# Optimization experiments

Hardware: AMD Instinct MI355X
Metric: run time of the kernel (lower is better)

## Reference

```python
import jax, jax.numpy as jnp
import numpy as np

DIM = 1024


def setup_inputs() -> dict:
    key = jax.random.key(0)
    k1, k2, k3 = jax.random.split(key, 3)
    B, N, D = 8, 2048, DIM
    feature1 = jax.random.normal(k1, (B, N, D), dtype=jnp.float32)
    feature2 = jax.random.normal(k2, (B, N, D), dtype=jnp.float32)
    # torch nn.Linear(dim, 3*dim, bias=False); stored here as [D, 3D] for x @ W
    W_qkv = jax.random.normal(k3, (D, 3 * D), dtype=jnp.float32) * (1.0 / np.sqrt(D))
    return {"feature1": feature1, "feature2": feature2, "W_qkv": W_qkv, "topk": 16}


def _qkv(x, W):
    b, n, d = x.shape
    qkv = (x @ W).reshape(b, n, 3, d)  # [B,N,3,D]
    q, k, v = qkv[:, :, 0], qkv[:, :, 1], qkv[:, :, 2]
    return q, k, v


def _topk_renorm(attn, topk):
    # attn: [B,N,N] row-softmax. Keep top-k per row, renormalize by row-sum of
    # the PRE-mask attention (which is 1.0 — faithful to the original code).
    b, n, _ = attn.shape
    _, idx = jax.lax.top_k(attn, topk)  # idx: [B,N,topk]
    bi = jnp.arange(b)[:, None, None]
    ri = jnp.arange(n)[None, :, None]
    mask = jnp.zeros_like(attn).at[bi, ri, idx].set(1.0)
    denom = jnp.sum(attn, axis=2)[:, :, None]  # [B,N,1], == 1 after softmax
    return attn * mask / denom


def reference(feature1, feature2, W_qkv, topk):
    d = feature1.shape[-1]
    scale = 1.0 / d ** 0.5
    q1, k1, v1 = _qkv(feature1, W_qkv)
    q2, k2, v2 = _qkv(feature2, W_qkv)
    dot1 = jnp.einsum("bqd,bkd->bqk", q1, k2) * scale
    dot2 = jnp.einsum("bqd,bkd->bqk", q2, k1) * scale
    attn1 = jax.nn.softmax(dot1, axis=-1)
    attn2 = jax.nn.softmax(dot2, axis=-1)
    attn1 = _topk_renorm(attn1, topk)
    attn2 = _topk_renorm(attn2, topk)
    feature_2to1 = jnp.einsum("bqk,bkd->bqd", attn1, v2)
    feature_1to2 = jnp.einsum("bqk,bkd->bqd", attn2, v1)
    return (feature_2to1, feature_1to2)
```

## Files before the change

kernel.cpp:

```cpp
#include <hip/hip_runtime.h>
#include <hip/hip_bf16.h>
#include <math.h>


#define SEQ 2048
#define DIMD 1024
#define NCAND 24

typedef __bf16 bf16x8 __attribute__((ext_vector_type(8)));
typedef float f32x4 __attribute__((ext_vector_type(4)));

__device__ __forceinline__ void split1(float x, unsigned short& h, unsigned short& l)
{
    __hip_bfloat16 hb = __float2bfloat16(x);
    float hf = __bfloat162float(hb);
    __hip_bfloat16 lb = __float2bfloat16(x - hf);
    h = *reinterpret_cast<unsigned short*>(&hb);
    l = *reinterpret_cast<unsigned short*>(&lb);
}

__global__ __launch_bounds__(256) void k_gemm_m(const float* __restrict__ W,
                                                double* __restrict__ M)
{
    __shared__ double As[16][65];
    __shared__ double Bs[16][65];
    const int tid = threadIdx.x;
    const int tx = tid & 15, ty = tid >> 4;
    const int m0 = blockIdx.x * 64, n0 = blockIdx.y * 64;
    const int lr = tid >> 2;
    const int lk = (tid & 3) * 4;
    double acc[4][4] = {};
    for (int k0 = 0; k0 < 1024; k0 += 16) {
        float4 a = *(const float4*)(W + (size_t)(m0 + lr) * 3072 + k0 + lk);
        As[lk+0][lr] = a.x; As[lk+1][lr] = a.y; As[lk+2][lr] = a.z; As[lk+3][lr] = a.w;
        float4 b = *(const float4*)(W + (size_t)(n0 + lr) * 3072 + 1024 + k0 + lk);
        Bs[lk+0][lr] = b.x; Bs[lk+1][lr] = b.y; Bs[lk+2][lr] = b.z; Bs[lk+3][lr] = b.w;
        __syncthreads();
        #pragma unroll
        for (int kk = 0; kk < 16; ++kk) {
            double av[4], bv[4];
            #pragma unroll
            for (int i = 0; i < 4; ++i) av[i] = As[kk][ty*4+i];
            #pragma unroll
            for (int j = 0; j < 4; ++j) bv[j] = Bs[kk][tx*4+j];
            #pragma unroll
            for (int i = 0; i < 4; ++i)
                #pragma unroll
                for (int j = 0; j < 4; ++j)
                    acc[i][j] = fma(av[i], bv[j], acc[i][j]);
        }
        __syncthreads();
    }
    #pragma unroll
    for (int i = 0; i < 4; ++i)
        #pragma unroll
        for (int j = 0; j < 4; ++j)
            M[(size_t)(m0 + ty*4 + i) * 1024 + n0 + tx*4 + j] = acc[i][j];
}

__global__ __launch_bounds__(256) void k_gemm_y64(const float* __restrict__ X,
                                                  const double* __restrict__ M,
                                                  double* __restrict__ Yd,
                                                  unsigned short* __restrict__ Yh,
                                                  unsigned short* __restrict__ Yl)
{
    __shared__ double As[16][65];
    __shared__ double Bs[16][65];
    const int tid = threadIdx.x;
    const int tx = tid & 15, ty = tid >> 4;
    const int m0 = blockIdx.x * 64, n0 = blockIdx.y * 64;
    const int lr = tid >> 2;
    const int lk = (tid & 3) * 4;
    const int bk = tid >> 4;
    const int bn = (tid & 15) * 4;
    double acc[4][4] = {};
    for (int k0 = 0; k0 < 1024; k0 += 16) {
        float4 a = *(const float4*)(X + (size_t)(m0 + lr) * 1024 + k0 + lk);
        As[lk+0][lr] = a.x; As[lk+1][lr] = a.y; As[lk+2][lr] = a.z; As[lk+3][lr] = a.w;
        const double* pb = M + (size_t)(k0 + bk) * 1024 + n0 + bn;
        double2 b01 = *(const double2*)pb;
        double2 b23 = *(const double2*)(pb + 2);
        Bs[bk][bn+0] = b01.x; Bs[bk][bn+1] = b01.y; Bs[bk][bn+2] = b23.x; Bs[bk][bn+3] = b23.y;
        __syncthreads();
        #pragma unroll
        for (int kk = 0; kk < 16; ++kk) {
            double av[4], bv[4];
            #pragma unroll
            for (int i = 0; i < 4; ++i) av[i] = As[kk][ty + 16*i];
            #pragma unroll
            for (int j = 0; j < 4; ++j) bv[j] = Bs[kk][tx + 16*j];
            #pragma unroll
            for (int i = 0; i < 4; ++i)
                #pragma unroll
                for (int j = 0; j < 4; ++j)
                    acc[i][j] = fma(av[i], bv[j], acc[i][j]);
        }
        __syncthreads();
    }
    #pragma unroll
    for (int i = 0; i < 4; ++i)
        #pragma unroll
        for (int j = 0; j < 4; ++j) {
            const double y = acc[i][j];
            const size_t o = (size_t)(m0 + ty + 16*i) * 1024 + n0 + tx + 16*j;
            Yd[o] = y;
            float yf = (float)y;
            __hip_bfloat16 hb = __float2bfloat16(yf);
            float hf = __bfloat162float(hb);
            __hip_bfloat16 lb = __float2bfloat16((float)(y - (double)hf));
            Yh[o] = *reinterpret_cast<unsigned short*>(&hb);
            Yl[o] = *reinterpret_cast<unsigned short*>(&lb);
        }
}

__global__ __launch_bounds__(256) void k_wvt_split(const float* __restrict__ W,
                                                   unsigned short* __restrict__ Th,
                                                   unsigned short* __restrict__ Tl)
{
    __shared__ float T[64][65];
    const int tid = threadIdx.x;
    const int tx = tid & 15, ty = tid >> 4;
    const int c0 = blockIdx.x * 64;
    const int n0 = blockIdx.y * 64;
    #pragma unroll
    for (int i = 0; i < 4; ++i) {
        float4 v = *(const float4*)(W + (size_t)(c0 + ty + 16*i) * 3072 + 2048 + n0 + tx*4);
        T[ty+16*i][tx*4+0] = v.x; T[ty+16*i][tx*4+1] = v.y;
        T[ty+16*i][tx*4+2] = v.z; T[ty+16*i][tx*4+3] = v.w;
    }
    __syncthreads();
    #pragma unroll
    for (int i = 0; i < 4; ++i) {
        const int n = ty + 16*i;
        ushort4 hh, ll; unsigned short h, l;
        split1(T[tx*4+0][n], h, l); hh.x = h; ll.x = l;
        split1(T[tx*4+1][n], h, l); hh.y = h; ll.y = l;
        split1(T[tx*4+2][n], h, l); hh.z = h; ll.z = l;
        split1(T[tx*4+3][n], h, l); hh.w = h; ll.w = l;
        size_t o = (size_t)(n0 + n) * 1024 + c0 + tx*4;
        *(ushort4*)(Th + o) = hh;
        *(ushort4*)(Tl + o) = ll;
    }
}

__global__ __launch_bounds__(256) void k_split4(const float4* __restrict__ x,
                                                ushort4* __restrict__ h4,
                                                ushort4* __restrict__ l4)
{
    const int i = blockIdx.x * 256 + threadIdx.x;
    float4 v = x[i];
    ushort4 hh, ll; unsigned short h, l;
    split1(v.x, h, l); hh.x = h; ll.x = l;
    split1(v.y, h, l); hh.y = h; ll.y = l;
    split1(v.z, h, l); hh.z = h; ll.z = l;
    split1(v.w, h, l); hh.w = h; ll.w = l;
    h4[i] = hh; l4[i] = ll;
}

__global__ __launch_bounds__(256) void k_mfma_split(
    const unsigned short* __restrict__ Ah, const unsigned short* __restrict__ Al,
    const unsigned short* __restrict__ Bh, const unsigned short* __restrict__ Bl,
    float* __restrict__ C, int N, float scale)
{
    __shared__ __align__(16) unsigned short sAh[128][32];
    __shared__ __align__(16) unsigned short sAl[128][32];
    __shared__ __align__(16) unsigned short sBh[128][32];
    __shared__ __align__(16) unsigned short sBl[128][32];
    const int tid  = threadIdx.x;
    const int lane = tid & 63;
    const int wid  = tid >> 6;
    const int wm = wid >> 1, wn = wid & 1;
    const int ar0 = blockIdx.x * 128;
    const int br0 = blockIdx.y * 128;

    f32x4 acc[4][4] = {};

    const int srow = lane >> 2;
    const int scol = (lane & 3) * 8;
    const int fr   = lane & 15;
    const int kg   = (lane >> 4) * 8;

    for (int k0 = 0; k0 < 1024; k0 += 32) {
        #pragma unroll
        for (int cc = 0; cc < 2; ++cc) {
            const int c = wid + cc * 4;
            const size_t gA = (size_t)(ar0 + c*16 + srow) * 1024 + k0 + scol;
            const size_t gB = (size_t)(br0 + c*16 + srow) * 1024 + k0 + scol;
            __builtin_amdgcn_global_load_lds((const __attribute__((address_space(1))) void*)(Ah + gA),
                (__attribute__((address_space(3))) void*)((char*)&sAh[0][0] + c*1024), 16, 0, 0);
            __builtin_amdgcn_global_load_lds((const __attribute__((address_space(1))) void*)(Al + gA),
                (__attribute__((address_space(3))) void*)((char*)&sAl[0][0] + c*1024), 16, 0, 0);
            __builtin_amdgcn_global_load_lds((const __attribute__((address_space(1))) void*)(Bh + gB),
                (__attribute__((address_space(3))) void*)((char*)&sBh[0][0] + c*1024), 16, 0, 0);
            __builtin_amdgcn_global_load_lds((const __attribute__((address_space(1))) void*)(Bl + gB),
                (__attribute__((address_space(3))) void*)((char*)&sBl[0][0] + c*1024), 16, 0, 0);
        }
        __syncthreads();

        bf16x8 aH[4], aL[4], bH[4], bL[4];
        #pragma unroll
        for (int i = 0; i < 4; ++i) {
            aH[i] = *(const bf16x8*)&sAh[wm*64 + i*16 + fr][kg];
            aL[i] = *(const bf16x8*)&sAl[wm*64 + i*16 + fr][kg];
            bH[i] = *(const bf16x8*)&sBh[wn*64 + i*16 + fr][kg];
            bL[i] = *(const bf16x8*)&sBl[wn*64 + i*16 + fr][kg];
        }
        #pragma unroll
        for (int mi = 0; mi < 4; ++mi)
            #pragma unroll
            for (int ni = 0; ni < 4; ++ni) {
                acc[mi][ni] = __builtin_amdgcn_mfma_f32_16x16x32_bf16(aH[mi], bH[ni], acc[mi][ni], 0, 0, 0);
                acc[mi][ni] = __builtin_amdgcn_mfma_f32_16x16x32_bf16(aH[mi], bL[ni], acc[mi][ni], 0, 0, 0);
                acc[mi][ni] = __builtin_amdgcn_mfma_f32_16x16x32_bf16(aL[mi], bH[ni], acc[mi][ni], 0, 0, 0);
            }
        __syncthreads();
    }

    const int rsub = (lane >> 4) * 4;
    const int csub = lane & 15;
    const int orow0 = ar0 + wm*64;
    const int ocol0 = br0 + wn*64;
    #pragma unroll
    for (int mi = 0; mi < 4; ++mi)
        #pragma unroll
        for (int ni = 0; ni < 4; ++ni)
            #pragma unroll
            for (int r = 0; r < 4; ++r)
                C[(size_t)(orow0 + mi*16 + rsub + r) * N + ocol0 + ni*16 + csub] = acc[mi][ni][r] * scale;
}

__global__ __launch_bounds__(256) void k_topk_out(const float* __restrict__ Z,
                                                  const float* __restrict__ V,
                                                  const double* __restrict__ Yd,
                                                  const float* __restrict__ Xo,
                                                  float* __restrict__ out)
{
    __shared__ float  zrow[SEQ];
    __shared__ double yrow[DIMD];
    __shared__ float  rvf[256];
    __shared__ int    ri[256];
    __shared__ double rvd[256];
    __shared__ double zc[NCAND];
    __shared__ int    ci[NCAND];
    __shared__ float  selw[16];
    __shared__ int    seli[16];
    __shared__ float  szmax, szsum;
    const int tid = threadIdx.x;
    const int row = blockIdx.x;

    const float* zr = Z + (size_t)row * SEQ;
    for (int i = tid; i < SEQ; i += 256) zrow[i] = zr[i];
    const double* yr = Yd + (size_t)row * DIMD;
    for (int i = tid; i < DIMD; i += 256) yrow[i] = yr[i];
    __syncthreads();

    float mv = -3.0e38f;
    for (int i = tid; i < SEQ; i += 256) mv = fmaxf(mv, zrow[i]);
    rvf[tid] = mv; __syncthreads();
    for (int s = 128; s; s >>= 1) { if (tid < s) rvf[tid] = fmaxf(rvf[tid], rvf[tid+s]); __syncthreads(); }
    if (tid == 0) szmax = rvf[0];
    __syncthreads();
    const float zmax = szmax;

    float ls = 0.f;
    for (int i = tid; i < SEQ; i += 256) ls += expf(zrow[i] - zmax);
    rvf[tid] = ls; __syncthreads();
    for (int s = 128; s; s >>= 1) { if (tid < s) rvf[tid] += rvf[tid+s]; __syncthreads(); }
    if (tid == 0) szsum = rvf[0];
    __syncthreads();

    for (int t = 0; t < NCAND; ++t) {
        float bvv = -3.0e38f; int bii = 1 << 30;
        for (int i = tid; i < SEQ; i += 256) {
            float v = zrow[i];
            if (v > bvv || (v == bvv && i < bii)) { bvv = v; bii = i; }
        }
        rvf[tid] = bvv; ri[tid] = bii; __syncthreads();
        for (int s = 128; s; s >>= 1) {
            if (tid < s) {
                float ov = rvf[tid+s]; int oi = ri[tid+s];
                if (ov > rvf[tid] || (ov == rvf[tid] && oi < ri[tid])) { rvf[tid] = ov; ri[tid] = oi; }
            }
            __syncthreads();
        }
        if (tid == 0) { ci[t] = ri[0]; zrow[ri[0]] = -3.0e38f; }
        __syncthreads();
    }

    for (int t = 0; t < NCAND; ++t) {
        const float* xc = Xo + (size_t)ci[t] * DIMD;
        double s = 0.0;
        for (int i = tid; i < DIMD; i += 256) s = fma(yrow[i], (double)xc[i], s);
        rvd[tid] = s; __syncthreads();
        for (int s2 = 128; s2; s2 >>= 1) { if (tid < s2) rvd[tid] += rvd[tid+s2]; __syncthreads(); }
        if (tid == 0) zc[t] = rvd[0] * 0.03125;
        __syncthreads();
    }

    if (tid == 0) {
        bool used[NCAND] = {};
        for (int t = 0; t < 16; ++t) {
            double bv = -1.0e300; int bj = -1;
            for (int j = 0; j < NCAND; ++j) {
                if (used[j]) continue;
                if (bj < 0 || zc[j] > bv || (zc[j] == bv && ci[j] < ci[bj])) { bv = zc[j]; bj = j; }
            }
            used[bj] = true;
            seli[t] = ci[bj];
            selw[t] = (float)exp(bv - (double)zmax);
        }
    }
    __syncthreads();

    float w[16]; int idx[16];
    #pragma unroll
    for (int j = 0; j < 16; ++j) { w[j] = selw[j]; idx[j] = seli[j]; }
    const float invZ = 1.0f / szsum;
    float* orow = out + (size_t)row * DIMD;
    for (int d = tid; d < DIMD; d += 256) {
        float acc = 0.f;
        #pragma unroll
        for (int j = 0; j < 16; ++j)
            acc = fmaf(w[j], V[(size_t)idx[j] * DIMD + d], acc);
        orow[d] = acc * invZ;
    }
}

extern "C" void kernel_launch(void* const* d_in, const int* in_sizes, int n_in,
                              void* d_out, int out_size, void* d_ws, size_t ws_size,
                              hipStream_t stream)
{
    const float* X1 = (const float*)d_in[0];
    const float* X2 = (const float*)d_in[1];
    const float* W  = (const float*)d_in[2];
    float* out = (float*)d_out;

    char* ws = (char*)d_ws;
    const size_t MB = 1ull << 20;
    double*         M   = (double*)(ws);
    unsigned short* Wvh = (unsigned short*)(ws +  8*MB);
    unsigned short* Wvl = (unsigned short*)(ws + 10*MB);
    unsigned short* Xsh = (unsigned short*)(ws + 12*MB);
    unsigned short* Xsl = (unsigned short*)(ws + 16*MB);
    double*         Yd  = (double*)(ws + 20*MB);
    unsigned short* Yh  = (unsigned short*)(ws + 36*MB);
    unsigned short* Yl  = (unsigned short*)(ws + 40*MB);
    float*          V   = (float*)(ws + 36*MB);
    float*          Z   = (float*)(ws + 44*MB);

    const size_t XB   = (size_t)SEQ * DIMD;
    const size_t OUTH = (size_t)8 * SEQ * DIMD;

    dim3 blk(256);
    k_gemm_m<<<dim3(16, 16), blk, 0, stream>>>(W, M);
    k_wvt_split<<<dim3(16, 16), blk, 0, stream>>>(W, Wvh, Wvl);

    for (int b = 0; b < 8; ++b) {
        const float* x1 = X1 + (size_t)b * XB;
        const float* x2 = X2 + (size_t)b * XB;

        k_split4<<<dim3(2048), blk, 0, stream>>>((const float4*)x2, (ushort4*)Xsh, (ushort4*)Xsl);
        k_gemm_y64<<<dim3(32, 16), blk, 0, stream>>>(x1, M, Yd, Yh, Yl);
        k_mfma_split<<<dim3(16, 16), blk, 0, stream>>>(Yh, Yl, Xsh, Xsl, Z, 2048, 0.03125f);
        k_mfma_split<<<dim3(16,  8), blk, 0, stream>>>(Xsh, Xsl, Wvh, Wvl, V, 1024, 1.0f);
        k_topk_out<<<dim3(SEQ), blk, 0, stream>>>(Z, V, Yd, x2, out + (size_t)b * XB);

        k_split4<<<dim3(2048), blk, 0, stream>>>((const float4*)x1, (ushort4*)Xsh, (ushort4*)Xsl);
        k_gemm_y64<<<dim3(32, 16), blk, 0, stream>>>(x2, M, Yd, Yh, Yl);
        k_mfma_split<<<dim3(16, 16), blk, 0, stream>>>(Yh, Yl, Xsh, Xsl, Z, 2048, 0.03125f);
        k_mfma_split<<<dim3(16,  8), blk, 0, stream>>>(Xsh, Xsl, Wvh, Wvl, V, 1024, 1.0f);
        k_topk_out<<<dim3(SEQ), blk, 0, stream>>>(Z, V, Yd, x1, out + OUTH + (size_t)b * XB);
    }
}
```

Before: 8.509 ms.

## Use register-resident scores and wavefront shuffles for top-k candidate selection

The top-k kernel keeps each row's 2048 scores in registers, eight per thread, instead of shared memory. It replaces the shared-memory tree reductions (eight barriers each) with wave-level xor-shuffle reductions plus a small cross-wave merge. Each of the 24 candidate-extraction steps now needs one barrier, and only the owning thread rescans its eight values. The candidate dot products are split across waves, one wave per candidate, with a shuffle reduction. This trades more register use and a double-buffered reduction slot for far fewer barriers and less shared-memory traffic.

```diff
diff --git a/kernel.cpp b/kernel.cpp
--- a/kernel.cpp
+++ b/kernel.cpp
@@ -235,67 +235,103 @@
                                                   const float* __restrict__ Xo,
                                                   float* __restrict__ out)
 {
-    __shared__ float  zrow[SEQ];
     __shared__ double yrow[DIMD];
-    __shared__ float  rvf[256];
-    __shared__ int    ri[256];
-    __shared__ double rvd[256];
+    __shared__ float  redv[8];
+    __shared__ int    redi[8];
+    __shared__ float  sums[4];
     __shared__ double zc[NCAND];
-    __shared__ int    ci[NCAND];
     __shared__ float  selw[16];
     __shared__ int    seli[16];
-    __shared__ float  szmax, szsum;
-    const int tid = threadIdx.x;
-    const int row = blockIdx.x;
+    const int tid  = threadIdx.x;
+    const int lane = tid & 63;
+    const int wid  = tid >> 6;
+    const int row  = blockIdx.x;
 
     const float* zr = Z + (size_t)row * SEQ;
-    for (int i = tid; i < SEQ; i += 256) zrow[i] = zr[i];
+    float zv[8];
+    #pragma unroll
+    for (int j = 0; j < 8; ++j) zv[j] = zr[tid + 256*j];
+
     const double* yr = Yd + (size_t)row * DIMD;
     for (int i = tid; i < DIMD; i += 256) yrow[i] = yr[i];
+
+    float lmax = -3.0e38f; int lidx = 1 << 30;
+    #pragma unroll
+    for (int j = 0; j < 8; ++j)
+        if (zv[j] > lmax) { lmax = zv[j]; lidx = tid + 256*j; }
+
+    {
+        float v = lmax; int gi = lidx;
+        #pragma unroll
+        for (int off = 32; off; off >>= 1) {
+            float ov = __shfl_xor(v, off);
+            int   oi = __shfl_xor(gi, off);
+            if (ov > v || (ov == v && oi < gi)) { v = ov; gi = oi; }
+        }
+        if (lane == 0) { redv[wid] = v; redi[wid] = gi; }
+    }
     __syncthreads();
-
-    float mv = -3.0e38f;
-    for (int i = tid; i < SEQ; i += 256) mv = fmaxf(mv, zrow[i]);
-    rvf[tid] = mv; __syncthreads();
-    for (int s = 128; s; s >>= 1) { if (tid < s) rvf[tid] = fmaxf(rvf[tid], rvf[tid+s]); __syncthreads(); }
-    if (tid == 0) szmax = rvf[0];
+    float zmax;
+    {
+        float v = redv[0];
+        #pragma unroll
+        for (int w = 1; w < 4; ++w) if (redv[w] > v) v = redv[w];
+        zmax = v;
+    }
+
+    {
+        float ls = 0.f;
+        #pragma unroll
+        for (int j = 0; j < 8; ++j) ls += expf(zv[j] - zmax);
+        #pragma unroll
+        for (int off = 32; off; off >>= 1) ls += __shfl_xor(ls, off);
+        if (lane == 0) sums[wid] = ls;
+    }
     __syncthreads();
-    const float zmax = szmax;
-
-    float ls = 0.f;
-    for (int i = tid; i < SEQ; i += 256) ls += expf(zrow[i] - zmax);
-    rvf[tid] = ls; __syncthreads();
-    for (int s = 128; s; s >>= 1) { if (tid < s) rvf[tid] += rvf[tid+s]; __syncthreads(); }
-    if (tid == 0) szsum = rvf[0];
+    const float szsum = sums[0] + sums[1] + sums[2] + sums[3];
+
+    int cand[NCAND];
+    for (int t = 0; t < NCAND; ++t) {
+        float v = lmax; int gi = lidx;
+        #pragma unroll
+        for (int off = 32; off; off >>= 1) {
+            float ov = __shfl_xor(v, off);
+            int   oi = __shfl_xor(gi, off);
+            if (ov > v || (ov == v && oi < gi)) { v = ov; gi = oi; }
+        }
+        const int slot = (t & 1) * 4;
+        if (lane == 0) { redv[slot + wid] = v; redi[slot + wid] = gi; }
+        __syncthreads();
+        {
+            float bv = redv[slot]; int bi = redi[slot];
+            #pragma unroll
+            for (int w = 1; w < 4; ++w) {
+                float ov = redv[slot + w]; int oi = redi[slot + w];
+                if (ov > bv || (ov == bv && oi < bi)) { bv = ov; bi = oi; }
+            }
+            cand[t] = bi;
+            if ((bi & 255) == tid) {
+                zv[bi >> 8] = -3.0e38f;
+                lmax = -3.0e38f; lidx = 1 << 30;
+                #pragma unroll
+                for (int j = 0; j < 8; ++j)
+                    if (zv[j] > lmax) { lmax = zv[j]; lidx = tid + 256*j; }
+            }
+        }
+    }
+
+    for (int s = 0; s < NCAND / 4; ++s) {
+        const int t = wid + 4 * s;
+        const float* xc = Xo + (size_t)cand[t] * DIMD;
+        double acc = 0.0;
+        #pragma unroll
+        for (int e = 0; e < 16; ++e)
+            acc = fma(yrow[e*64 + lane], (double)xc[e*64 + lane], acc);
+        #pragma unroll
+        for (int off = 32; off; off >>= 1) acc += __shfl_xor(acc, off);
+        if (lane == 0) zc[t] = acc * 0.03125;
+    }
     __syncthreads();
-
-    for (int t = 0; t < NCAND; ++t) {
-        float bvv = -3.0e38f; int bii = 1 << 30;
-        for (int i = tid; i < SEQ; i += 256) {
-            float v = zrow[i];
-            if (v > bvv || (v == bvv && i < bii)) { bvv = v; bii = i; }
-        }
-        rvf[tid] = bvv; ri[tid] = bii; __syncthreads();
-        for (int s = 128; s; s >>= 1) {
-            if (tid < s) {
-                float ov = rvf[tid+s]; int oi = ri[tid+s];
-                if (ov > rvf[tid] || (ov == rvf[tid] && oi < ri[tid])) { rvf[tid] = ov; ri[tid] = oi; }
-            }
-            __syncthreads();
-        }
-        if (tid == 0) { ci[t] = ri[0]; zrow[ri[0]] = -3.0e38f; }
-        __syncthreads();
-    }
-
-    for (int t = 0; t < NCAND; ++t) {
-        const float* xc = Xo + (size_t)ci[t] * DIMD;
-        double s = 0.0;
-        for (int i = tid; i < DIMD; i += 256) s = fma(yrow[i], (double)xc[i], s);
-        rvd[tid] = s; __syncthreads();
-        for (int s2 = 128; s2; s2 >>= 1) { if (tid < s2) rvd[tid] += rvd[tid+s2]; __syncthreads(); }
-        if (tid == 0) zc[t] = rvd[0] * 0.03125;
-        __syncthreads();
-    }
 
     if (tid == 0) {
         bool used[NCAND] = {};
@@ -303,10 +339,10 @@
             double bv = -1.0e300; int bj = -1;
             for (int j = 0; j < NCAND; ++j) {
                 if (used[j]) continue;
-                if (bj < 0 || zc[j] > bv || (zc[j] == bv && ci[j] < ci[bj])) { bv = zc[j]; bj = j; }
+                if (bj < 0 || zc[j] > bv || (zc[j] == bv && cand[j] < cand[bj])) { bv = zc[j]; bj = j; }
             }
             used[bj] = true;
-            seli[t] = ci[bj];
+            seli[t] = cand[bj];
             selw[t] = (float)exp(bv - (double)zmax);
         }
     }
@@ -317,7 +353,9 @@
     for (int j = 0; j < 16; ++j) { w[j] = selw[j]; idx[j] = seli[j]; }
     const float invZ = 1.0f / szsum;
     float* orow = out + (size_t)row * DIMD;
-    for (int d = tid; d < DIMD; d += 256) {
+    #pragma unroll
+    for (int jj = 0; jj < 4; ++jj) {
+        const int d = tid + 256 * jj;
         float acc = 0.f;
         #pragma unroll
         for (int j = 0; j < 16; ++j)
```

Result: faster. 7.542 ms (-11.4%).
